# Performance work log

Measured on AMD Instinct MI355X. Metric: run time of the kernel, lower is better.

Reference implementation:

```python
import jax, jax.numpy as jnp
import numpy as np

N_NODES = 100000
N_EDGES = 1600000
D_IN = 128
D_HID = 128
N_LAYERS = 3


def setup_inputs() -> dict:
    key = jax.random.key(0)
    k1, k2, k3, k4 = jax.random.split(key, 4)
    x = jax.random.normal(k1, (N_NODES, D_IN), dtype=jnp.float32)
    edge_index = jax.random.randint(k2, (2, N_EDGES), 0, N_NODES, dtype=jnp.int64)
    # Glorot-ish scale for stability across 3 layers
    Ws = jax.random.normal(k3, (N_LAYERS, D_IN, D_HID), dtype=jnp.float32) * (1.0 / np.sqrt(D_IN))
    bs = jax.random.normal(k4, (N_LAYERS, D_HID), dtype=jnp.float32) * 0.01
    return {"x": x, "edge_index": edge_index, "Ws": Ws, "bs": bs}


def _gcn_conv(x, row, col, deg_inv_sqrt, W, b, n_nodes):
    # Linear transform first (PyG GCNConv), then gather-normalize-scatter.
    h = x @ W                                        # [N, D]
    norm = deg_inv_sqrt[row] * deg_inv_sqrt[col]     # [E+N] (self-loops included)
    msg = h[row] * norm[:, None]                     # gather + scale, [E+N, D]
    out = jax.ops.segment_sum(msg, col, num_segments=n_nodes)  # scatter-add
    return out + b


def reference(x, edge_index, Ws, bs):
    n = x.shape[0]
    # add self-loops once (same for every layer)
    loop = jnp.arange(n, dtype=edge_index.dtype)
    row = jnp.concatenate([edge_index[0], loop])
    col = jnp.concatenate([edge_index[1], loop])
    # symmetric normalization: deg over target nodes (incl. self-loops)
    deg = jax.ops.segment_sum(jnp.ones_like(col, dtype=x.dtype), col, num_segments=n)
    deg_inv_sqrt = jnp.where(deg > 0, jax.lax.rsqrt(jnp.maximum(deg, 1.0)), 0.0)
    h = x
    for i in range(Ws.shape[0]):
        h = jax.nn.relu(_gcn_conv(h, row, col, deg_inv_sqrt, Ws[i], bs[i], n))
    return h
```

## Files before the change

### kernel.cpp

```cpp
#include <hip/hip_runtime.h>
#include <hip/hip_bf16.h>

#define NN 100000
#define NE 1600000
#define DD 128
#define NBUK 196
#define F1_BLOCKS 256
#define F3_BLOCKS 256

typedef unsigned short ushort_t;
typedef unsigned int uint_t;
typedef __attribute__((ext_vector_type(8))) short bf16x8;
typedef __attribute__((ext_vector_type(4))) float f32x4;

__device__ __forceinline__ ushort_t bf16rne(float f) {
    uint_t u = __float_as_uint(f);
    u += 0x7FFF + ((u >> 16) & 1);
    return (ushort_t)(u >> 16);
}
__device__ __forceinline__ float bfLo(uint_t u) { return __uint_as_float(u << 16); }
__device__ __forceinline__ float bfHi(uint_t u) { return __uint_as_float(u & 0xFFFF0000u); }


__global__ __launch_bounds__(256) void f1_bucket_count(const int* __restrict__ col,
                                                       int* __restrict__ bukCount) {
    __shared__ int hist[NBUK];
    for (int t = threadIdx.x; t < NBUK; t += 256) hist[t] = 0;
    __syncthreads();
    const int epb = (NE + F1_BLOCKS - 1) / F1_BLOCKS;
    const int e0 = blockIdx.x * epb;
    const int e1 = min(e0 + epb, NE);
    for (int e = e0 + threadIdx.x; e < e1; e += 256)
        atomicAdd(&hist[col[e] >> 9], 1);
    __syncthreads();
    for (int t = threadIdx.x; t < NBUK; t += 256)
        if (hist[t]) atomicAdd(&bukCount[t], hist[t]);
}

__global__ void f2_bucket_scan(const int* __restrict__ bukCount,
                               int* __restrict__ bukBase,
                               int* __restrict__ bukCursor,
                               int* __restrict__ offsets) {
    __shared__ int s[256];
    const int t = threadIdx.x;
    int v = (t < NBUK) ? bukCount[t] : 0;
    s[t] = v;
    __syncthreads();
    for (int off = 1; off < 256; off <<= 1) {
        int tmp = (t >= off) ? s[t - off] : 0;
        __syncthreads();
        s[t] += tmp;
        __syncthreads();
    }
    int excl = s[t] - v;
    if (t < NBUK) { bukBase[t] = excl; bukCursor[t] = excl; }
    if (t == 255) { bukBase[NBUK] = s[255]; offsets[NN] = s[255]; }
}

__global__ __launch_bounds__(256) void f3_scatter(const int* __restrict__ row,
                                                  const int* __restrict__ col,
                                                  int* __restrict__ bukCursor,
                                                  int2* __restrict__ ebuf) {
    __shared__ int hist[NBUK];
    __shared__ int base[NBUK];
    __shared__ int rnk[NBUK];
    for (int t = threadIdx.x; t < NBUK; t += 256) { hist[t] = 0; rnk[t] = 0; }
    __syncthreads();
    const int epb = (NE + F3_BLOCKS - 1) / F3_BLOCKS;
    const int e0 = blockIdx.x * epb;
    const int e1 = min(e0 + epb, NE);
    for (int e = e0 + threadIdx.x; e < e1; e += 256)
        atomicAdd(&hist[col[e] >> 9], 1);
    __syncthreads();
    for (int t = threadIdx.x; t < NBUK; t += 256)
        base[t] = hist[t] ? atomicAdd(&bukCursor[t], hist[t]) : 0;
    __syncthreads();
    for (int e = e0 + threadIdx.x; e < e1; e += 256) {
        int c = col[e];
        int b = c >> 9;
        int r = atomicAdd(&rnk[b], 1);
        ebuf[base[b] + r] = make_int2(row[e], c);
    }
}

__global__ __launch_bounds__(256) void f4_finalize(const int2* __restrict__ ebuf,
                                                   const int* __restrict__ bukBase,
                                                   int* __restrict__ offsets,
                                                   float* __restrict__ dis,
                                                   int* __restrict__ csr_src) {
    __shared__ int cnt[512];
    __shared__ int cur[512];
    __shared__ int s[256];
    const int t = threadIdx.x;
    const int colBase = blockIdx.x << 9;
    const int ncols = min(512, NN - colBase);
    cnt[t] = 0; cnt[t + 256] = 0;
    __syncthreads();
    const int eb0 = bukBase[blockIdx.x];
    const int eb1 = bukBase[blockIdx.x + 1];
    for (int e = eb0 + t; e < eb1; e += 256)
        atomicAdd(&cnt[ebuf[e].y - colBase], 1);
    __syncthreads();
    const int c0 = cnt[2 * t], c1 = cnt[2 * t + 1];
    const int psum = c0 + c1;
    s[t] = psum;
    __syncthreads();
    for (int off = 1; off < 256; off <<= 1) {
        int tmp = (t >= off) ? s[t - off] : 0;
        __syncthreads();
        s[t] += tmp;
        __syncthreads();
    }
    const int exclPair = s[t] - psum;
    const int g0 = eb0 + exclPair;
    const int g1 = g0 + c0;
    cur[2 * t] = g0; cur[2 * t + 1] = g1;
    if (2 * t < ncols)     { offsets[colBase + 2 * t]     = g0; dis[colBase + 2 * t]     = rsqrtf((float)(c0 + 1)); }
    if (2 * t + 1 < ncols) { offsets[colBase + 2 * t + 1] = g1; dis[colBase + 2 * t + 1] = rsqrtf((float)(c1 + 1)); }
    __syncthreads();
    for (int e = eb0 + t; e < eb1; e += 256) {
        int2 rc = ebuf[e];
        int p = atomicAdd(&cur[rc.y - colBase], 1);
        csr_src[p] = rc.x;
    }
}


__global__ __launch_bounds__(256) void wt_kernel(const float* __restrict__ Ws,
                                                 ushort_t* __restrict__ wT) {
    int idx = blockIdx.x * 256 + threadIdx.x;
    if (idx >= 3 * 128 * 16) return;
    int l = idx >> 11;
    int r = idx & 2047;
    int c = r >> 4;
    int kc = r & 15;
    const float* w = Ws + l * 16384;
    ushort_t tmp[8];
#pragma unroll
    for (int e = 0; e < 8; ++e)
        tmp[e] = bf16rne(w[(kc * 8 + e) * 128 + c]);
    *(uint4*)&wT[(size_t)l * 16384 + c * 128 + kc * 8] = *(uint4*)tmp;
}


template<bool XF32>
__global__ __launch_bounds__(256) void gemm_mfma(const void* __restrict__ Xv,
                                                 const ushort_t* __restrict__ wT,
                                                 const float* __restrict__ dis,
                                                 ushort_t* __restrict__ Y) {
    __shared__ short wlds[128 * 136];
    {
        const uint4* src = (const uint4*)wT;
        int t = threadIdx.x;
#pragma unroll
        for (int i = 0; i < 8; ++i) {
            int idx = i * 256 + t;
            int rowc = idx >> 4;
            int kc = idx & 15;
            uint4 v = src[idx];
            *(uint4*)&wlds[rowc * 136 + kc * 8] = v;
        }
    }
    __syncthreads();

    const int wave = threadIdx.x >> 6;
    const int lane = threadIdx.x & 63;
    const int m = lane & 15;
    const int kg = lane >> 4;
    const int r0 = blockIdx.x * 64 + wave * 16;
    const int rowA = min(r0 + m, NN - 1);

    f32x4 acc[8];
#pragma unroll
    for (int ct = 0; ct < 8; ++ct) acc[ct] = (f32x4){0.f, 0.f, 0.f, 0.f};

#pragma unroll
    for (int ks = 0; ks < 4; ++ks) {
        bf16x8 af;
        if (XF32) {
            const float* xp = (const float*)Xv + (size_t)rowA * DD + ks * 32 + kg * 8;
            float4 f0 = *(const float4*)xp;
            float4 f1 = *(const float4*)(xp + 4);
            af[0] = (short)bf16rne(f0.x); af[1] = (short)bf16rne(f0.y);
            af[2] = (short)bf16rne(f0.z); af[3] = (short)bf16rne(f0.w);
            af[4] = (short)bf16rne(f1.x); af[5] = (short)bf16rne(f1.y);
            af[6] = (short)bf16rne(f1.z); af[7] = (short)bf16rne(f1.w);
        } else {
            const ushort_t* xp = (const ushort_t*)Xv + (size_t)rowA * DD + ks * 32 + kg * 8;
            af = *(const bf16x8*)xp;
        }
#pragma unroll
        for (int ct = 0; ct < 8; ++ct) {
            bf16x8 bf = *(const bf16x8*)&wlds[(ct * 16 + m) * 136 + ks * 32 + kg * 8];
            acc[ct] = __builtin_amdgcn_mfma_f32_16x16x32_bf16(af, bf, acc[ct], 0, 0, 0);
        }
    }

    const int rbase = r0 + kg * 4;
    float dv[4];
#pragma unroll
    for (int rg = 0; rg < 4; ++rg) dv[rg] = dis[min(rbase + rg, NN - 1)];
#pragma unroll
    for (int ct = 0; ct < 8; ++ct) {
#pragma unroll
        for (int rg = 0; rg < 4; ++rg) {
            int row = rbase + rg;
            if (row < NN)
                Y[(size_t)row * DD + ct * 16 + m] = bf16rne(acc[ct][rg] * dv[rg]);
        }
    }
}


template<bool F32OUT>
__global__ __launch_bounds__(256) void agg_kernel(const uint_t* __restrict__ lin2,
                                                  const int* __restrict__ offsets,
                                                  const int* __restrict__ csr_src,
                                                  const float* __restrict__ dis,
                                                  const float* __restrict__ bias,
                                                  void* __restrict__ outv) {
    const int wave = threadIdx.x >> 6;
    const int lane = threadIdx.x & 63;
    const int v = blockIdx.x * 4 + wave;

    const int start = offsets[v];
    const int end   = offsets[v + 1];
    const int n     = end - start;
    const int nv    = n < 64 ? n : 64;

    int idxv = 0;
    if (lane < nv) idxv = csr_src[start + lane];

    const float dv = dis[v];
    uint_t self = lin2[(size_t)v * 64 + lane];
    float2 b    = ((const float2*)bias)[lane];

    float accx = 0.f, accy = 0.f;
    int k = 0;
    for (; k + 8 <= nv; k += 8) {
        int s0 = __shfl(idxv, k + 0);
        int s1 = __shfl(idxv, k + 1);
        int s2 = __shfl(idxv, k + 2);
        int s3 = __shfl(idxv, k + 3);
        int s4 = __shfl(idxv, k + 4);
        int s5 = __shfl(idxv, k + 5);
        int s6 = __shfl(idxv, k + 6);
        int s7 = __shfl(idxv, k + 7);
        uint_t a0 = lin2[(size_t)s0 * 64 + lane];
        uint_t a1 = lin2[(size_t)s1 * 64 + lane];
        uint_t a2 = lin2[(size_t)s2 * 64 + lane];
        uint_t a3 = lin2[(size_t)s3 * 64 + lane];
        uint_t a4 = lin2[(size_t)s4 * 64 + lane];
        uint_t a5 = lin2[(size_t)s5 * 64 + lane];
        uint_t a6 = lin2[(size_t)s6 * 64 + lane];
        uint_t a7 = lin2[(size_t)s7 * 64 + lane];
        accx += bfLo(a0) + bfLo(a1) + bfLo(a2) + bfLo(a3)
              + bfLo(a4) + bfLo(a5) + bfLo(a6) + bfLo(a7);
        accy += bfHi(a0) + bfHi(a1) + bfHi(a2) + bfHi(a3)
              + bfHi(a4) + bfHi(a5) + bfHi(a6) + bfHi(a7);
    }
    for (; k + 4 <= nv; k += 4) {
        int s0 = __shfl(idxv, k + 0);
        int s1 = __shfl(idxv, k + 1);
        int s2 = __shfl(idxv, k + 2);
        int s3 = __shfl(idxv, k + 3);
        uint_t a0 = lin2[(size_t)s0 * 64 + lane];
        uint_t a1 = lin2[(size_t)s1 * 64 + lane];
        uint_t a2 = lin2[(size_t)s2 * 64 + lane];
        uint_t a3 = lin2[(size_t)s3 * 64 + lane];
        accx += bfLo(a0) + bfLo(a1) + bfLo(a2) + bfLo(a3);
        accy += bfHi(a0) + bfHi(a1) + bfHi(a2) + bfHi(a3);
    }
    for (; k < nv; ++k) {
        int s = __shfl(idxv, k);
        uint_t a = lin2[(size_t)s * 64 + lane];
        accx += bfLo(a); accy += bfHi(a);
    }
    for (int e = start + 64; e < end; ++e) {
        int s = csr_src[e];
        uint_t a = lin2[(size_t)s * 64 + lane];
        accx += bfLo(a); accy += bfHi(a);
    }

    float rx = fmaxf(dv * (accx + bfLo(self)) + b.x, 0.f);
    float ry = fmaxf(dv * (accy + bfHi(self)) + b.y, 0.f);
    if (F32OUT) {
        ((float2*)outv)[(size_t)v * 64 + lane] = make_float2(rx, ry);
    } else {
        uint_t pk = (uint_t)bf16rne(rx) | ((uint_t)bf16rne(ry) << 16);
        ((uint_t*)outv)[(size_t)v * 64 + lane] = pk;
    }
}


extern "C" void kernel_launch(void* const* d_in, const int* in_sizes, int n_in,
                              void* d_out, int out_size, void* d_ws, size_t ws_size,
                              hipStream_t stream) {
    const float* x   = (const float*)d_in[0];
    const int*   ei  = (const int*)d_in[1];
    const float* Ws  = (const float*)d_in[2];
    const float* bs  = (const float*)d_in[3];

    const int* row = ei;
    const int* col = ei + NE;

    char* ws = (char*)d_ws;
    ushort_t* lin    = (ushort_t*)(ws + 0);
    int2*  ebuf      = (int2*) (ws + 0);
    ushort_t* hb     = (ushort_t*)(ws + 25600000);
    float* dis       = (float*)(ws + 51200000);
    int*   offsets   = (int*)  (ws + 51600000);
    int*   csr_src   = (int*)  (ws + 52000016);
    int*   bukCount  = (int*)  (ws + 58400016);
    int*   bukBase   = (int*)  (ws + 58400800);
    int*   bukCursor = (int*)  (ws + 58401600);
    ushort_t* wT     = (ushort_t*)(ws + 58402432);

    hipMemsetAsync(bukCount, 0, NBUK * sizeof(int), stream);
    f1_bucket_count<<<F1_BLOCKS, 256, 0, stream>>>(col, bukCount);
    f2_bucket_scan<<<1, 256, 0, stream>>>(bukCount, bukBase, bukCursor, offsets);
    f3_scatter<<<F3_BLOCKS, 256, 0, stream>>>(row, col, bukCursor, ebuf);
    f4_finalize<<<NBUK, 256, 0, stream>>>(ebuf, bukBase, offsets, dis, csr_src);
    wt_kernel<<<24, 256, 0, stream>>>(Ws, wT);

    const int gemmGrid = (NN + 63) / 64;
    gemm_mfma<true><<<gemmGrid, 256, 0, stream>>>(x, wT, dis, lin);
    agg_kernel<false><<<NN / 4, 256, 0, stream>>>((const uint_t*)lin, offsets, csr_src, dis, bs, hb);
    gemm_mfma<false><<<gemmGrid, 256, 0, stream>>>(hb, wT + 16384, dis, lin);
    agg_kernel<false><<<NN / 4, 256, 0, stream>>>((const uint_t*)lin, offsets, csr_src, dis, bs + DD, hb);
    gemm_mfma<false><<<gemmGrid, 256, 0, stream>>>(hb, wT + 32768, dis, lin);
    agg_kernel<true><<<NN / 4, 256, 0, stream>>>((const uint_t*)lin, offsets, csr_src, dis, bs + 2 * DD, d_out);
}
```

Before: 306.1 us.

## Split agg features across XCDs, pack edge buffer, per-wave scatter histograms

The aggregation kernel now handles two nodes per wave, 32 lanes each. The feature dimension is split in half by XCD (block id bits), so each XCD gathers only half of every row, which is meant to improve L2 locality of the gathered lin rows. Outputs use nontemporal stores. The CSR build packs (row<<9 | col&511) into a single int to halve ebuf traffic, and f3_scatter uses per-wave shared histograms to cut LDS atomic contention. In exchange, each wave does half-width 128-byte gathers with predicated accumulation, and the node-to-block mapping depends on the hardware's round-robin XCD assignment.

Measured after the change: 291.9 us. 4.6% less time.

```diff
diff --git a/kernel.cpp b/kernel.cpp
--- a/kernel.cpp
+++ b/kernel.cpp
@@ -60,30 +60,41 @@
 __global__ __launch_bounds__(256) void f3_scatter(const int* __restrict__ row,
                                                   const int* __restrict__ col,
                                                   int* __restrict__ bukCursor,
-                                                  int2* __restrict__ ebuf) {
-    __shared__ int hist[NBUK];
-    __shared__ int base[NBUK];
-    __shared__ int rnk[NBUK];
-    for (int t = threadIdx.x; t < NBUK; t += 256) { hist[t] = 0; rnk[t] = 0; }
+                                                  int* __restrict__ ebuf) {
+    __shared__ int hist[4][NBUK];
+    __shared__ int base[4][NBUK];
+    const int t = threadIdx.x;
+    const int w = t >> 6;
+    const int lane = t & 63;
+    for (int i = t; i < 4 * NBUK; i += 256) (&hist[0][0])[i] = 0;
     __syncthreads();
     const int epb = (NE + F3_BLOCKS - 1) / F3_BLOCKS;
     const int e0 = blockIdx.x * epb;
     const int e1 = min(e0 + epb, NE);
-    for (int e = e0 + threadIdx.x; e < e1; e += 256)
-        atomicAdd(&hist[col[e] >> 9], 1);
-    __syncthreads();
-    for (int t = threadIdx.x; t < NBUK; t += 256)
-        base[t] = hist[t] ? atomicAdd(&bukCursor[t], hist[t]) : 0;
-    __syncthreads();
-    for (int e = e0 + threadIdx.x; e < e1; e += 256) {
+    const int wepb = (e1 - e0 + 3) >> 2;
+    const int we0 = e0 + w * wepb;
+    const int we1 = min(we0 + wepb, e1);
+    for (int e = we0 + lane; e < we1; e += 64)
+        atomicAdd(&hist[w][col[e] >> 9], 1);
+    __syncthreads();
+    if (t < NBUK) {
+        int h0 = hist[0][t], h1 = hist[1][t], h2 = hist[2][t], h3 = hist[3][t];
+        int tot = h0 + h1 + h2 + h3;
+        int g = tot ? atomicAdd(&bukCursor[t], tot) : 0;
+        base[0][t] = g; base[1][t] = g + h0;
+        base[2][t] = g + h0 + h1; base[3][t] = g + h0 + h1 + h2;
+        hist[0][t] = 0; hist[1][t] = 0; hist[2][t] = 0; hist[3][t] = 0;
+    }
+    __syncthreads();
+    for (int e = we0 + lane; e < we1; e += 64) {
         int c = col[e];
         int b = c >> 9;
-        int r = atomicAdd(&rnk[b], 1);
-        ebuf[base[b] + r] = make_int2(row[e], c);
-    }
-}
-
-__global__ __launch_bounds__(256) void f4_finalize(const int2* __restrict__ ebuf,
+        int r = atomicAdd(&hist[w][b], 1);
+        ebuf[base[w][b] + r] = (row[e] << 9) | (c & 511);
+    }
+}
+
+__global__ __launch_bounds__(256) void f4_finalize(const int* __restrict__ ebuf,
                                                    const int* __restrict__ bukBase,
                                                    int* __restrict__ offsets,
                                                    float* __restrict__ dis,
@@ -99,7 +110,7 @@
     const int eb0 = bukBase[blockIdx.x];
     const int eb1 = bukBase[blockIdx.x + 1];
     for (int e = eb0 + t; e < eb1; e += 256)
-        atomicAdd(&cnt[ebuf[e].y - colBase], 1);
+        atomicAdd(&cnt[ebuf[e] & 511], 1);
     __syncthreads();
     const int c0 = cnt[2 * t], c1 = cnt[2 * t + 1];
     const int psum = c0 + c1;
@@ -119,9 +130,9 @@
     if (2 * t + 1 < ncols) { offsets[colBase + 2 * t + 1] = g1; dis[colBase + 2 * t + 1] = rsqrtf((float)(c1 + 1)); }
     __syncthreads();
     for (int e = eb0 + t; e < eb1; e += 256) {
-        int2 rc = ebuf[e];
-        int p = atomicAdd(&cur[rc.y - colBase], 1);
-        csr_src[p] = rc.x;
+        int pc = ebuf[e];
+        int p = atomicAdd(&cur[pc & 511], 1);
+        csr_src[p] = pc >> 9;
     }
 }
 
@@ -219,76 +230,75 @@
                                                   const float* __restrict__ dis,
                                                   const float* __restrict__ bias,
                                                   void* __restrict__ outv) {
-    const int wave = threadIdx.x >> 6;
+    const int bid = blockIdx.x;
+    const int xcd = bid & 7;
+    const int h   = (xcd >> 2);
+    const int g   = (bid >> 3) * 4 + (xcd & 3);
+    const int w    = threadIdx.x >> 6;
     const int lane = threadIdx.x & 63;
-    const int v = blockIdx.x * 4 + wave;
+    const int l32  = lane & 31;
+    const int hi   = lane >> 5;
+    const int v = g * 8 + w * 2 + hi;
 
     const int start = offsets[v];
     const int end   = offsets[v + 1];
     const int n     = end - start;
-    const int nv    = n < 64 ? n : 64;
+    const int nvm   = n < 32 ? n : 32;
 
     int idxv = 0;
-    if (lane < nv) idxv = csr_src[start + lane];
-
+    if (l32 < nvm) idxv = csr_src[start + l32];
+
+    const int nv_other = __shfl(nvm, lane ^ 32);
+    const int kmax = nvm > nv_other ? nvm : nv_other;
+
+    const int doff = h * 32 + l32;
     const float dv = dis[v];
-    uint_t self = lin2[(size_t)v * 64 + lane];
-    float2 b    = ((const float2*)bias)[lane];
+    uint_t self = lin2[(size_t)v * 64 + doff];
+    float2 b    = ((const float2*)bias)[doff];
 
     float accx = 0.f, accy = 0.f;
-    int k = 0;
-    for (; k + 8 <= nv; k += 8) {
-        int s0 = __shfl(idxv, k + 0);
-        int s1 = __shfl(idxv, k + 1);
-        int s2 = __shfl(idxv, k + 2);
-        int s3 = __shfl(idxv, k + 3);
-        int s4 = __shfl(idxv, k + 4);
-        int s5 = __shfl(idxv, k + 5);
-        int s6 = __shfl(idxv, k + 6);
-        int s7 = __shfl(idxv, k + 7);
-        uint_t a0 = lin2[(size_t)s0 * 64 + lane];
-        uint_t a1 = lin2[(size_t)s1 * 64 + lane];
-        uint_t a2 = lin2[(size_t)s2 * 64 + lane];
-        uint_t a3 = lin2[(size_t)s3 * 64 + lane];
-        uint_t a4 = lin2[(size_t)s4 * 64 + lane];
-        uint_t a5 = lin2[(size_t)s5 * 64 + lane];
-        uint_t a6 = lin2[(size_t)s6 * 64 + lane];
-        uint_t a7 = lin2[(size_t)s7 * 64 + lane];
-        accx += bfLo(a0) + bfLo(a1) + bfLo(a2) + bfLo(a3)
-              + bfLo(a4) + bfLo(a5) + bfLo(a6) + bfLo(a7);
-        accy += bfHi(a0) + bfHi(a1) + bfHi(a2) + bfHi(a3)
-              + bfHi(a4) + bfHi(a5) + bfHi(a6) + bfHi(a7);
-    }
-    for (; k + 4 <= nv; k += 4) {
-        int s0 = __shfl(idxv, k + 0);
-        int s1 = __shfl(idxv, k + 1);
-        int s2 = __shfl(idxv, k + 2);
-        int s3 = __shfl(idxv, k + 3);
-        uint_t a0 = lin2[(size_t)s0 * 64 + lane];
-        uint_t a1 = lin2[(size_t)s1 * 64 + lane];
-        uint_t a2 = lin2[(size_t)s2 * 64 + lane];
-        uint_t a3 = lin2[(size_t)s3 * 64 + lane];
-        accx += bfLo(a0) + bfLo(a1) + bfLo(a2) + bfLo(a3);
-        accy += bfHi(a0) + bfHi(a1) + bfHi(a2) + bfHi(a3);
-    }
-    for (; k < nv; ++k) {
-        int s = __shfl(idxv, k);
-        uint_t a = lin2[(size_t)s * 64 + lane];
-        accx += bfLo(a); accy += bfHi(a);
-    }
-    for (int e = start + 64; e < end; ++e) {
+    const int sbase = (lane & 32);
+    for (int k = 0; k < kmax; k += 8) {
+        int s0 = __shfl(idxv, sbase + k + 0);
+        int s1 = __shfl(idxv, sbase + k + 1);
+        int s2 = __shfl(idxv, sbase + k + 2);
+        int s3 = __shfl(idxv, sbase + k + 3);
+        int s4 = __shfl(idxv, sbase + k + 4);
+        int s5 = __shfl(idxv, sbase + k + 5);
+        int s6 = __shfl(idxv, sbase + k + 6);
+        int s7 = __shfl(idxv, sbase + k + 7);
+        uint_t a0 = lin2[(size_t)s0 * 64 + doff];
+        uint_t a1 = lin2[(size_t)s1 * 64 + doff];
+        uint_t a2 = lin2[(size_t)s2 * 64 + doff];
+        uint_t a3 = lin2[(size_t)s3 * 64 + doff];
+        uint_t a4 = lin2[(size_t)s4 * 64 + doff];
+        uint_t a5 = lin2[(size_t)s5 * 64 + doff];
+        uint_t a6 = lin2[(size_t)s6 * 64 + doff];
+        uint_t a7 = lin2[(size_t)s7 * 64 + doff];
+        if (k + 0 < nvm) { accx += bfLo(a0); accy += bfHi(a0); }
+        if (k + 1 < nvm) { accx += bfLo(a1); accy += bfHi(a1); }
+        if (k + 2 < nvm) { accx += bfLo(a2); accy += bfHi(a2); }
+        if (k + 3 < nvm) { accx += bfLo(a3); accy += bfHi(a3); }
+        if (k + 4 < nvm) { accx += bfLo(a4); accy += bfHi(a4); }
+        if (k + 5 < nvm) { accx += bfLo(a5); accy += bfHi(a5); }
+        if (k + 6 < nvm) { accx += bfLo(a6); accy += bfHi(a6); }
+        if (k + 7 < nvm) { accx += bfLo(a7); accy += bfHi(a7); }
+    }
+    for (int e = start + 32; e < end; ++e) {
         int s = csr_src[e];
-        uint_t a = lin2[(size_t)s * 64 + lane];
+        uint_t a = lin2[(size_t)s * 64 + doff];
         accx += bfLo(a); accy += bfHi(a);
     }
 
     float rx = fmaxf(dv * (accx + bfLo(self)) + b.x, 0.f);
     float ry = fmaxf(dv * (accy + bfHi(self)) + b.y, 0.f);
+    const size_t oidx = (size_t)v * 64 + doff;
     if (F32OUT) {
-        ((float2*)outv)[(size_t)v * 64 + lane] = make_float2(rx, ry);
+        float2 o = make_float2(rx, ry);
+        __builtin_nontemporal_store(*(const double*)&o, (double*)((float2*)outv + oidx));
     } else {
         uint_t pk = (uint_t)bf16rne(rx) | ((uint_t)bf16rne(ry) << 16);
-        ((uint_t*)outv)[(size_t)v * 64 + lane] = pk;
+        __builtin_nontemporal_store(pk, (uint_t*)outv + oidx);
     }
 }
 
@@ -306,7 +316,7 @@
 
     char* ws = (char*)d_ws;
     ushort_t* lin    = (ushort_t*)(ws + 0);
-    int2*  ebuf      = (int2*) (ws + 0);
+    int*   ebuf      = (int*)  (ws + 0);
     ushort_t* hb     = (ushort_t*)(ws + 25600000);
     float* dis       = (float*)(ws + 51200000);
     int*   offsets   = (int*)  (ws + 51600000);
@@ -324,10 +334,11 @@
     wt_kernel<<<24, 256, 0, stream>>>(Ws, wT);
 
     const int gemmGrid = (NN + 63) / 64;
+    const int aggGrid = (NN / 8) * 2;
     gemm_mfma<true><<<gemmGrid, 256, 0, stream>>>(x, wT, dis, lin);
-    agg_kernel<false><<<NN / 4, 256, 0, stream>>>((const uint_t*)lin, offsets, csr_src, dis, bs, hb);
+    agg_kernel<false><<<aggGrid, 256, 0, stream>>>((const uint_t*)lin, offsets, csr_src, dis, bs, hb);
     gemm_mfma<false><<<gemmGrid, 256, 0, stream>>>(hb, wT + 16384, dis, lin);
-    agg_kernel<false><<<NN / 4, 256, 0, stream>>>((const uint_t*)lin, offsets, csr_src, dis, bs + DD, hb);
+    agg_kernel<false><<<aggGrid, 256, 0, stream>>>((const uint_t*)lin, offsets, csr_src, dis, bs + DD, hb);
     gemm_mfma<false><<<gemmGrid, 256, 0, stream>>>(hb, wT + 32768, dis, lin);
-    agg_kernel<true><<<NN / 4, 256, 0, stream>>>((const uint_t*)lin, offsets, csr_src, dis, bs + 2 * DD, d_out);
-}
+    agg_kernel<true><<<aggGrid, 256, 0, stream>>>((const uint_t*)lin, offsets, csr_src, dis, bs + 2 * DD, d_out);
+}
```
